# Kernel optimization log

Measured on AMD Instinct MI355X. Metric: run time of the kernel, lower is better.

The kernel has to match this reference:

```python
import jax, jax.numpy as jnp
import numpy as np

EPS_NORM = 1e-12  # torch F.normalize eps
EPS_LOG = 1e-6


def _l2_normalize(x, axis):
    n = jnp.linalg.norm(x, axis=axis, keepdims=True)
    return x / jnp.maximum(n, EPS_NORM)


def setup_inputs() -> dict:
    key = jax.random.key(0)
    k1, k2, k3 = jax.random.split(key, 3)
    B, C, D = 32, 5000, 512
    features = jax.random.normal(k1, (B, C, D), dtype=jnp.float32)
    embeddings = jax.random.normal(k2, (C, D), dtype=jnp.float32)
    labels = jax.random.randint(k3, (B, C), 0, 2).astype(jnp.float32)
    return {"features": features, "embeddings": embeddings, "labels": labels}


def reference(features, embeddings, labels):
    # features: (B, C, D), embeddings: (C, D), labels: (B, C)
    C = embeddings.shape[0]
    fn = _l2_normalize(features, axis=2)
    en = _l2_normalize(embeddings, axis=1)
    # diagonal of bmm(fn, en^T) == row-wise dot products: (B, C)
    similarities = jnp.einsum('bcd,cd->bc', fn, en)
    S = (1.0 + similarities) / 2.0 + EPS_LOG
    pos_loss = labels * jnp.log(S)
    neg_loss = (1.0 - labels) * jnp.log(
        1.0 - (C - 1) / C * jnp.abs(1.0 / (C - 1) + similarities) + EPS_LOG
    )
    return -(pos_loss + neg_loss).mean()
```

## Files before the change

kernel.cpp:

```cpp
#include <hip/hip_runtime.h>
#include <math.h>


typedef float f32x4 __attribute__((ext_vector_type(4)));

constexpr int B = 32;
constexpr int C = 5000;
constexpr int D = 512;
constexpr int NROWS = B * C;
constexpr float EPS_LOG = 1e-6f;

constexpr int WPB = 4;
constexpr int THREADS = WPB * 64;
constexpr int NBLOCKS = 1280;
constexpr int NWAVES_TOT = NBLOCKS * WPB;
constexpr int QROWS = 8;
constexpr int UNITS = NROWS / QROWS;

__global__ __launch_bounds__(THREADS) void fll_main(
    const float* __restrict__ feat,
    const float* __restrict__ emb,
    const float* __restrict__ labels,
    float* __restrict__ partial)
{
    const int lane = threadIdx.x & 63;
    const int wid  = threadIdx.x >> 6;
    const int gw   = blockIdx.x * WPB + wid;

    const size_t bstr = (size_t)C * D;
    float wacc = 0.0f;

    for (int u = gw; u < UNITS; u += NWAVES_TOT) {
        const int c = u >> 2;
        const int q = u & 3;

        const f32x4* er = reinterpret_cast<const f32x4*>(emb + (size_t)c * D);
        const f32x4 e0 = er[lane];
        const f32x4 e1 = er[lane + 64];
        float ess = e0.x * e0.x + e0.y * e0.y + e0.z * e0.z + e0.w * e0.w
                  + e1.x * e1.x + e1.y * e1.y + e1.z * e1.z + e1.w * e1.w;
        #pragma unroll
        for (int off = 32; off > 0; off >>= 1) ess += __shfl_xor(ess, off, 64);

        const float* fb = feat + (size_t)(q * QROWS) * bstr + (size_t)c * D;
        const float* lb = labels + (size_t)(q * QROWS) * C + c;

        #pragma unroll 4
        for (int i = 0; i < QROWS; ++i) {
            const f32x4* fr = reinterpret_cast<const f32x4*>(fb + (size_t)i * bstr);
            const f32x4 f0 = fr[lane];
            const f32x4 f1 = fr[lane + 64];

            float dot = f0.x * e0.x + f0.y * e0.y + f0.z * e0.z + f0.w * e0.w
                      + f1.x * e1.x + f1.y * e1.y + f1.z * e1.z + f1.w * e1.w;
            float fss = f0.x * f0.x + f0.y * f0.y + f0.z * f0.z + f0.w * f0.w
                      + f1.x * f1.x + f1.y * f1.y + f1.z * f1.z + f1.w * f1.w;

            #pragma unroll
            for (int off = 32; off > 0; off >>= 1) {
                dot += __shfl_xor(dot, off, 64);
                fss += __shfl_xor(fss, off, 64);
            }

            const float sim = dot / sqrtf(fss * ess);
            const float lab = lb[(size_t)i * C];
            const float S = 0.5f * (1.0f + sim) + EPS_LOG;
            const float T = 1.0f
                - ((float)(C - 1) / (float)C) * fabsf(1.0f / (float)(C - 1) + sim)
                + EPS_LOG;
            wacc += logf(lab > 0.5f ? S : T);
        }
    }

    __shared__ float wsum[WPB];
    if (lane == 0) wsum[wid] = wacc;
    __syncthreads();
    if (threadIdx.x == 0) {
        float s = 0.0f;
        #pragma unroll
        for (int w = 0; w < WPB; ++w) s += wsum[w];
        partial[blockIdx.x] = s;
    }
}

__global__ __launch_bounds__(256) void fll_reduce(
    const float* __restrict__ partial, float* __restrict__ out)
{
    const int lane = threadIdx.x & 63;
    const int wave = threadIdx.x >> 6;
    double acc = 0.0;
    for (int i = threadIdx.x; i < NBLOCKS; i += 256) acc += (double)partial[i];

    #pragma unroll
    for (int off = 32; off > 0; off >>= 1) acc += __shfl_xor(acc, off, 64);

    __shared__ double s[4];
    if (lane == 0) s[wave] = acc;
    __syncthreads();
    if (threadIdx.x == 0) {
        double tot = 0.0;
        #pragma unroll
        for (int w = 0; w < 4; ++w) tot += s[w];
        out[0] = (float)(-tot / (double)NROWS);
    }
}

extern "C" void kernel_launch(void* const* d_in, const int* in_sizes, int n_in,
                              void* d_out, int out_size, void* d_ws, size_t ws_size,
                              hipStream_t stream) {
    const float* feat   = (const float*)d_in[0];
    const float* emb    = (const float*)d_in[1];
    const float* labels = (const float*)d_in[2];
    float* out = (float*)d_out;
    float* partial = (float*)d_ws;

    fll_main<<<NBLOCKS, THREADS, 0, stream>>>(feat, emb, labels, partial);
    fll_reduce<<<1, 256, 0, stream>>>(partial, out);
}
```

Before: 65.55 us.

## Stage embedding span in LDS and precompute inverse norms per block

Each block now handles a span of 10 classes for 4 batch rows. It first copies those embedding rows into shared memory and computes their inverse norms once, then each wave streams contiguous feature rows for one batch element. The aim is to cut the per-unit reloading and re-normalising of embeddings and to make feature reads sequential within a batch row. In exchange it launches 4000 blocks with a 20KB LDS tile, adds block-level syncs, and gives each wave only 10 rows of work, which may reduce latency hiding.

New measurement: 72.23 us. +10.2%, slower.

```diff
diff --git a/kernel.cpp b/kernel.cpp
--- a/kernel.cpp
+++ b/kernel.cpp
@@ -10,12 +10,12 @@
 constexpr int NROWS = B * C;
 constexpr float EPS_LOG = 1e-6f;
 
+constexpr int SPAN = 10;
+constexpr int NSPAN = C / SPAN;
 constexpr int WPB = 4;
 constexpr int THREADS = WPB * 64;
-constexpr int NBLOCKS = 1280;
-constexpr int NWAVES_TOT = NBLOCKS * WPB;
-constexpr int QROWS = 8;
-constexpr int UNITS = NROWS / QROWS;
+constexpr int BGROUPS = B / WPB;
+constexpr int NBLOCKS = NSPAN * BGROUPS;
 
 __global__ __launch_bounds__(THREADS) void fll_main(
     const float* __restrict__ feat,
@@ -23,63 +23,75 @@
     const float* __restrict__ labels,
     float* __restrict__ partial)
 {
-    const int lane = threadIdx.x & 63;
-    const int wid  = threadIdx.x >> 6;
-    const int gw   = blockIdx.x * WPB + wid;
+    __shared__ float tile[SPAN * D];
+    __shared__ float inv_ne[SPAN];
+    __shared__ float wsum[WPB];
 
-    const size_t bstr = (size_t)C * D;
+    const int t    = threadIdx.x;
+    const int lane = t & 63;
+    const int wid  = t >> 6;
+    const int bg   = blockIdx.x & 7;
+    const int s    = blockIdx.x >> 3;
+    const int b    = bg * WPB + wid;
+    const int c0   = s * SPAN;
+
+    const f32x4* esrc = reinterpret_cast<const f32x4*>(emb + (size_t)c0 * D);
+    f32x4* tl4 = reinterpret_cast<f32x4*>(tile);
+    #pragma unroll
+    for (int k = 0; k < (SPAN * D / 4) / THREADS; ++k)
+        tl4[t + k * THREADS] = esrc[t + k * THREADS];
+    __syncthreads();
+
+    for (int r = wid; r < SPAN; r += WPB) {
+        const f32x4 a0 = tl4[r * (D / 4) + lane];
+        const f32x4 a1 = tl4[r * (D / 4) + lane + 64];
+        float ss = a0.x * a0.x + a0.y * a0.y + a0.z * a0.z + a0.w * a0.w
+                 + a1.x * a1.x + a1.y * a1.y + a1.z * a1.z + a1.w * a1.w;
+        #pragma unroll
+        for (int off = 32; off > 0; off >>= 1) ss += __shfl_xor(ss, off, 64);
+        if (lane == 0) inv_ne[r] = 1.0f / sqrtf(ss);
+    }
+    __syncthreads();
+
+    const float* fbase = feat + ((size_t)b * C + c0) * D;
+    const float* lb    = labels + (size_t)b * C + c0;
     float wacc = 0.0f;
 
-    for (int u = gw; u < UNITS; u += NWAVES_TOT) {
-        const int c = u >> 2;
-        const int q = u & 3;
+    #pragma unroll 2
+    for (int r = 0; r < SPAN; ++r) {
+        const f32x4* fr = reinterpret_cast<const f32x4*>(fbase + (size_t)r * D);
+        const f32x4 f0 = fr[lane];
+        const f32x4 f1 = fr[lane + 64];
+        const f32x4 e0 = tl4[r * (D / 4) + lane];
+        const f32x4 e1 = tl4[r * (D / 4) + lane + 64];
 
-        const f32x4* er = reinterpret_cast<const f32x4*>(emb + (size_t)c * D);
-        const f32x4 e0 = er[lane];
-        const f32x4 e1 = er[lane + 64];
-        float ess = e0.x * e0.x + e0.y * e0.y + e0.z * e0.z + e0.w * e0.w
-                  + e1.x * e1.x + e1.y * e1.y + e1.z * e1.z + e1.w * e1.w;
+        float dot = f0.x * e0.x + f0.y * e0.y + f0.z * e0.z + f0.w * e0.w
+                  + f1.x * e1.x + f1.y * e1.y + f1.z * e1.z + f1.w * e1.w;
+        float fss = f0.x * f0.x + f0.y * f0.y + f0.z * f0.z + f0.w * f0.w
+                  + f1.x * f1.x + f1.y * f1.y + f1.z * f1.z + f1.w * f1.w;
+
         #pragma unroll
-        for (int off = 32; off > 0; off >>= 1) ess += __shfl_xor(ess, off, 64);
+        for (int off = 32; off > 0; off >>= 1) {
+            dot += __shfl_xor(dot, off, 64);
+            fss += __shfl_xor(fss, off, 64);
+        }
 
-        const float* fb = feat + (size_t)(q * QROWS) * bstr + (size_t)c * D;
-        const float* lb = labels + (size_t)(q * QROWS) * C + c;
-
-        #pragma unroll 4
-        for (int i = 0; i < QROWS; ++i) {
-            const f32x4* fr = reinterpret_cast<const f32x4*>(fb + (size_t)i * bstr);
-            const f32x4 f0 = fr[lane];
-            const f32x4 f1 = fr[lane + 64];
-
-            float dot = f0.x * e0.x + f0.y * e0.y + f0.z * e0.z + f0.w * e0.w
-                      + f1.x * e1.x + f1.y * e1.y + f1.z * e1.z + f1.w * e1.w;
-            float fss = f0.x * f0.x + f0.y * f0.y + f0.z * f0.z + f0.w * f0.w
-                      + f1.x * f1.x + f1.y * f1.y + f1.z * f1.z + f1.w * f1.w;
-
-            #pragma unroll
-            for (int off = 32; off > 0; off >>= 1) {
-                dot += __shfl_xor(dot, off, 64);
-                fss += __shfl_xor(fss, off, 64);
-            }
-
-            const float sim = dot / sqrtf(fss * ess);
-            const float lab = lb[(size_t)i * C];
-            const float S = 0.5f * (1.0f + sim) + EPS_LOG;
-            const float T = 1.0f
-                - ((float)(C - 1) / (float)C) * fabsf(1.0f / (float)(C - 1) + sim)
-                + EPS_LOG;
-            wacc += logf(lab > 0.5f ? S : T);
-        }
+        const float sim = dot * (1.0f / sqrtf(fss)) * inv_ne[r];
+        const float lab = lb[r];
+        const float S = 0.5f * (1.0f + sim) + EPS_LOG;
+        const float T = 1.0f
+            - ((float)(C - 1) / (float)C) * fabsf(1.0f / (float)(C - 1) + sim)
+            + EPS_LOG;
+        wacc += logf(lab > 0.5f ? S : T);
     }
 
-    __shared__ float wsum[WPB];
     if (lane == 0) wsum[wid] = wacc;
     __syncthreads();
-    if (threadIdx.x == 0) {
-        float s = 0.0f;
+    if (t == 0) {
+        float acc = 0.0f;
         #pragma unroll
-        for (int w = 0; w < WPB; ++w) s += wsum[w];
-        partial[blockIdx.x] = s;
+        for (int w = 0; w < WPB; ++w) acc += wsum[w];
+        partial[blockIdx.x] = acc;
     }
 }
 
@@ -94,13 +106,13 @@
     #pragma unroll
     for (int off = 32; off > 0; off >>= 1) acc += __shfl_xor(acc, off, 64);
 
-    __shared__ double s[4];
-    if (lane == 0) s[wave] = acc;
+    __shared__ double sd[4];
+    if (lane == 0) sd[wave] = acc;
     __syncthreads();
     if (threadIdx.x == 0) {
         double tot = 0.0;
         #pragma unroll
-        for (int w = 0; w < 4; ++w) tot += s[w];
+        for (int w = 0; w < 4; ++w) tot += sd[w];
         out[0] = (float)(-tot / (double)NROWS);
     }
 }
```
